# Kernel optimization log

Measured on AMD Instinct MI355X. Metric: run time of the kernel, lower is better.

Reference implementation:

```python
import jax, jax.numpy as jnp
import numpy as np

LOG_2PI = 1.8378770664093453  # log(2*pi)

B, N_FEAT = 4096, 1024
R, K, D = 64, 32, 16  # n_regions, n_batch (distributions per region), region size


def setup_inputs() -> dict:
    key = jax.random.key(0)
    k1, k2, k3, k4 = jax.random.split(key, 4)
    x = jax.random.normal(k1, (B, N_FEAT), dtype=jnp.float32)
    # Regions: partition-like index sets over the feature space (equal size D).
    regions = jax.random.randint(k2, (R, D), 0, N_FEAT, dtype=jnp.int64)
    # Per-region diag-Gaussian params (means ~ N(0, 0.1), scales near 1.0).
    means = 0.1 * jax.random.normal(k3, (R, K, D), dtype=jnp.float32)
    scales = 0.9 + 0.2 * jax.random.uniform(k4, (R, K, D), dtype=jnp.float32)
    return {"x": x, "regions": regions, "means": means, "scales": scales}


def reference(x, regions, means, scales):
    # Gather per-region features in one shot: [B, R, D]
    xg = x[:, regions]
    # Diag-Gaussian log-prob, broadcast over the K distributions per region.
    # z: [B, R, K, D]
    z = (xg[:, :, None, :] - means[None]) / scales[None]
    log_det = jnp.sum(jnp.log(scales), axis=-1)  # [R, K]
    ll = -0.5 * jnp.sum(z * z, axis=-1) - log_det[None] - 0.5 * D * LOG_2PI
    return ll  # [B, R, K] == stack over regions of MVNDiag.log_prob
```

## Files before the change

### kernel.cpp

```cpp
#include <hip/hip_runtime.h>

typedef __attribute__((ext_vector_type(8))) short short8;
typedef __attribute__((ext_vector_type(4))) float floatx4;

#define NB 4096
#define NF 1024
#define NR 64
#define NK 32
#define ND 16
#define HALF_D_LOG2PI 14.702988531274762f

__device__ __forceinline__ unsigned f2bf_bits(float f) {
    unsigned u = __float_as_uint(f);
    return (u + 0x7fffu + ((u >> 16) & 1u)) >> 16;
}
__device__ __forceinline__ float bf_bits2f(unsigned b) {
    return __uint_as_float(b << 16);
}

__global__ __launch_bounds__(256) void prep_kernel(
    const float* __restrict__ means, const float* __restrict__ scales,
    unsigned short* __restrict__ wfrag, float* __restrict__ cv)
{
    int p = blockIdx.x * 256 + threadIdx.x;
    if (p >= NR * NK) return;
    int n  = p & 15;
    int nt = (p >> 4) & 1;
    int r  = p >> 5;

    const float* m = means  + (size_t)p * ND;
    const float* s = scales + (size_t)p * ND;
    float Av[ND], Bv[ND];
    float csum = 0.f;
#pragma unroll
    for (int d = 0; d < ND; ++d) {
        float sd = s[d], md = m[d];
        float a  = 1.0f / sd;
        float a2 = a * a;
        Av[d] = -0.5f * a2;
        Bv[d] = md * a2;
        float c = md * a;
        csum += -0.5f * c * c - logf(sd);
    }
    cv[p] = csum - HALF_D_LOG2PI;

#pragma unroll
    for (int slot = 0; slot < 4; ++slot) {
        int ks = slot >> 1;
#pragma unroll
        for (int d = 0; d < ND; ++d) {
            int Kin  = (slot & 1) * 16 + d;
            int quad = Kin >> 3;
            int j    = Kin & 7;
            int lane = quad * 16 + n;
            size_t idx = ((((size_t)r * 2 + ks) * 2 + nt) * 64 + lane) * 8 + j;
            float v = (slot < 2) ? Av[d] : Bv[d];
            wfrag[idx] = (unsigned short)f2bf_bits(v);
        }
    }
}

__global__ __launch_bounds__(256, 2) void fused_kernel(
    const float* __restrict__ x, const int* __restrict__ regions,
    const unsigned short* __restrict__ wfrag, const float* __restrict__ cv,
    float* __restrict__ out)
{
    __shared__ __align__(16) char lds[16 * 1028 * 4 + 32 * 17 * 4];
    float* xs = (float*)lds;
    int*   ridx = (int*)(lds + 16 * 1028 * 4);
    unsigned short* xg = (unsigned short*)lds;

    const int t  = threadIdx.x;
    const int bt = blockIdx.x;
    const int r0 = blockIdx.y * 32;
    const int b0 = bt * 16;

    for (int j = t; j < 32 * ND; j += 256) {
        int rl = j >> 4, d = j & 15;
        ridx[rl * 17 + d] = regions[(r0 + rl) * ND + d];
    }
    {
        const float4* src = (const float4*)(x + (size_t)b0 * NF);
#pragma unroll
        for (int i = 0; i < 16; ++i)
            *(float4*)(xs + i * 1028 + t * 4) = src[i * 256 + t];
    }
    __syncthreads();

    const int rl = t & 31;
    const int bA = t >> 5;
    int idxv[ND];
#pragma unroll
    for (int d = 0; d < ND; ++d) idxv[d] = ridx[rl * 17 + d];

    unsigned pk[2][32];
#pragma unroll
    for (int pp = 0; pp < 2; ++pp) {
        const int b = bA + pp * 8;
#pragma unroll
        for (int d = 0; d < ND; d += 2) {
            float x0 = xs[b * 1028 + idxv[d]];
            float x1 = xs[b * 1028 + idxv[d + 1]];
            float q0 = x0 * x0, q1 = x1 * x1;
            unsigned h20 = f2bf_bits(q0), h21 = f2bf_bits(q1);
            unsigned l20 = f2bf_bits(q0 - bf_bits2f(h20));
            unsigned l21 = f2bf_bits(q1 - bf_bits2f(h21));
            unsigned h0  = f2bf_bits(x0), h1 = f2bf_bits(x1);
            unsigned l0  = f2bf_bits(x0 - bf_bits2f(h0));
            unsigned l1  = f2bf_bits(x1 - bf_bits2f(h1));
            int di = d >> 1;
            pk[pp][di]      = h20 | (h21 << 16);
            pk[pp][8 + di]  = l20 | (l21 << 16);
            pk[pp][16 + di] = h0  | (h1 << 16);
            pk[pp][24 + di] = l0  | (l1 << 16);
        }
    }
    __syncthreads();

    const int wv   = t >> 6;
    const int L    = t & 63;
    const int m    = L & 15;
    const int quad = L >> 4;
    const short* wfs = (const short*)wfrag;

#pragma unroll
    for (int c = 0; c < 2; ++c) {
        if ((rl >> 4) == c) {
            int rr = rl & 15;
#pragma unroll
            for (int pp = 0; pp < 2; ++pp) {
                int b = bA + pp * 8;
                uint4* d4 = (uint4*)(xg + (rr * 16 + b) * 72);
#pragma unroll
                for (int q = 0; q < 8; ++q) d4[q] = ((uint4*)pk[pp])[q];
            }
        }
        __syncthreads();

#pragma unroll
        for (int i = 0; i < 4; ++i) {
            int rloc = wv * 4 + i;
            int r    = r0 + c * 16 + rloc;
            const unsigned short* arow = xg + (rloc * 16 + m) * 72;
            short8 a0 = *(const short8*)(arow + quad * 8);
            short8 a1 = *(const short8*)(arow + 32 + quad * 8);

            size_t wb = ((size_t)r * 4) * 512 + (size_t)L * 8;
            short8 w00 = *(const short8*)(wfs + wb);
            short8 w01 = *(const short8*)(wfs + wb + 512);
            short8 w10 = *(const short8*)(wfs + wb + 1024);
            short8 w11 = *(const short8*)(wfs + wb + 1536);

            floatx4 acc0 = {0.f, 0.f, 0.f, 0.f};
            floatx4 acc1 = {0.f, 0.f, 0.f, 0.f};
            acc0 = __builtin_amdgcn_mfma_f32_16x16x32_bf16(a0, w00, acc0, 0, 0, 0);
            acc0 = __builtin_amdgcn_mfma_f32_16x16x32_bf16(a1, w10, acc0, 0, 0, 0);
            acc1 = __builtin_amdgcn_mfma_f32_16x16x32_bf16(a0, w01, acc1, 0, 0, 0);
            acc1 = __builtin_amdgcn_mfma_f32_16x16x32_bf16(a1, w11, acc1, 0, 0, 0);

            float c0 = cv[r * NK + m];
            float c1 = cv[r * NK + 16 + m];
            int brow = bt * 16 + quad * 4;
#pragma unroll
            for (int g = 0; g < 4; ++g) {
                size_t ob = (size_t)(brow + g) * (NR * NK) + (size_t)r * NK;
                out[ob + m]      = acc0[g] + c0;
                out[ob + 16 + m] = acc1[g] + c1;
            }
        }
        __syncthreads();
    }
}

extern "C" void kernel_launch(void* const* d_in, const int* in_sizes, int n_in,
                              void* d_out, int out_size, void* d_ws, size_t ws_size,
                              hipStream_t stream) {
    const float* x       = (const float*)d_in[0];
    const int*   regions = (const int*)d_in[1];
    const float* means   = (const float*)d_in[2];
    const float* scales  = (const float*)d_in[3];
    float* out = (float*)d_out;

    char* ws = (char*)d_ws;
    unsigned short* wfrag = (unsigned short*)ws;
    float*          cvp   = (float*)(ws + 262144);

    prep_kernel<<<dim3((NR * NK + 255) / 256), 256, 0, stream>>>(means, scales, wfrag, cvp);
    fused_kernel<<<dim3(NB / 16, 2), 256, 0, stream>>>(x, regions, wfrag, cvp, out);
}
```

Baseline: 90.00 us.

## Parallelize weight prep per region and swizzle single-pass LDS staging

The prep kernel now uses one block per region, staging A/B coefficients in shared memory, reducing the constant term cooperatively and writing the bf16 MFMA fragments as 16-byte vectors instead of scattered 2-byte stores. The fused kernel enlarges its LDS buffer so all 32 regions' gathered features are staged at once, removing the two-chunk loop and its extra barriers. Rows use an XOR swizzle to cut LDS bank conflicts on fragment reads. The larger LDS footprint may limit occupancy, and since the kernel is likely bound by output bandwidth the benefit may be limited.

```diff
diff --git a/kernel.cpp b/kernel.cpp
--- a/kernel.cpp
+++ b/kernel.cpp
@@ -22,42 +22,55 @@
     const float* __restrict__ means, const float* __restrict__ scales,
     unsigned short* __restrict__ wfrag, float* __restrict__ cv)
 {
-    int p = blockIdx.x * 256 + threadIdx.x;
-    if (p >= NR * NK) return;
-    int n  = p & 15;
-    int nt = (p >> 4) & 1;
-    int r  = p >> 5;
-
-    const float* m = means  + (size_t)p * ND;
-    const float* s = scales + (size_t)p * ND;
-    float Av[ND], Bv[ND];
-    float csum = 0.f;
-#pragma unroll
-    for (int d = 0; d < ND; ++d) {
-        float sd = s[d], md = m[d];
-        float a  = 1.0f / sd;
-        float a2 = a * a;
-        Av[d] = -0.5f * a2;
-        Bv[d] = md * a2;
-        float c = md * a;
-        csum += -0.5f * c * c - logf(sd);
-    }
-    cv[p] = csum - HALF_D_LOG2PI;
-
-#pragma unroll
-    for (int slot = 0; slot < 4; ++slot) {
-        int ks = slot >> 1;
-#pragma unroll
-        for (int d = 0; d < ND; ++d) {
-            int Kin  = (slot & 1) * 16 + d;
-            int quad = Kin >> 3;
-            int j    = Kin & 7;
-            int lane = quad * 16 + n;
-            size_t idx = ((((size_t)r * 2 + ks) * 2 + nt) * 64 + lane) * 8 + j;
-            float v = (slot < 2) ? Av[d] : Bv[d];
-            wfrag[idx] = (unsigned short)f2bf_bits(v);
-        }
-    }
+    __shared__ float Asm[NK][ND];
+    __shared__ float Bsm[NK][ND];
+    __shared__ float csum[NK][8];
+    const int r = blockIdx.x;
+    const int t = threadIdx.x;
+
+    {
+        int k  = t >> 3;
+        int d0 = (t & 7) * 2;
+        const float* m = means  + ((size_t)r * NK + k) * ND + d0;
+        const float* s = scales + ((size_t)r * NK + k) * ND + d0;
+        float partial = 0.f;
+#pragma unroll
+        for (int q = 0; q < 2; ++q) {
+            float sd = s[q], md = m[q];
+            float a  = 1.f / sd;
+            float a2 = a * a;
+            Asm[k][d0 + q] = -0.5f * a2;
+            Bsm[k][d0 + q] = md * a2;
+            float c = md * a;
+            partial += -0.5f * c * c - logf(sd);
+        }
+        csum[k][t & 7] = partial;
+    }
+    __syncthreads();
+    if (t < NK) {
+        float acc = 0.f;
+#pragma unroll
+        for (int q = 0; q < 8; ++q) acc += csum[t][q];
+        cv[r * NK + t] = acc - HALF_D_LOG2PI;
+    }
+
+    const int ks   = t >> 7;
+    const int nt   = (t >> 6) & 1;
+    const int lane = t & 63;
+    const int n    = lane & 15;
+    const int qd   = lane >> 4;
+    const int kk   = nt * 16 + n;
+    unsigned px[4];
+#pragma unroll
+    for (int j2 = 0; j2 < 4; ++j2) {
+        int j  = j2 * 2;
+        int d0 = (qd * 8 + j) & 15;
+        int d1 = (qd * 8 + j + 1) & 15;
+        float v0 = ks ? Bsm[kk][d0] : Asm[kk][d0];
+        float v1 = ks ? Bsm[kk][d1] : Asm[kk][d1];
+        px[j2] = f2bf_bits(v0) | (f2bf_bits(v1) << 16);
+    }
+    *(uint4*)(wfrag + ((((size_t)r * 2 + ks) * 2 + nt) * 64 + lane) * 8) = *(uint4*)px;
 }
 
 __global__ __launch_bounds__(256, 2) void fused_kernel(
@@ -65,8 +78,8 @@
     const unsigned short* __restrict__ wfrag, const float* __restrict__ cv,
     float* __restrict__ out)
 {
-    __shared__ __align__(16) char lds[16 * 1028 * 4 + 32 * 17 * 4];
-    float* xs = (float*)lds;
+    __shared__ __align__(16) char lds[73728];
+    float* xs   = (float*)lds;
     int*   ridx = (int*)(lds + 16 * 1028 * 4);
     unsigned short* xg = (unsigned short*)lds;
 
@@ -76,8 +89,8 @@
     const int b0 = bt * 16;
 
     for (int j = t; j < 32 * ND; j += 256) {
-        int rl = j >> 4, d = j & 15;
-        ridx[rl * 17 + d] = regions[(r0 + rl) * ND + d];
+        int rr = j >> 4, d = j & 15;
+        ridx[rr * 17 + d] = regions[(r0 + rr) * ND + d];
     }
     {
         const float4* src = (const float4*)(x + (size_t)b0 * NF);
@@ -117,58 +130,58 @@
     }
     __syncthreads();
 
+    {
+        const int s = rl & 7;
+#pragma unroll
+        for (int pp = 0; pp < 2; ++pp) {
+            int row = rl * 16 + bA + pp * 8;
+            uint4* base = (uint4*)(xg + row * 72);
+#pragma unroll
+            for (int q = 0; q < 8; ++q) base[q ^ s] = ((uint4*)pk[pp])[q];
+        }
+    }
+    __syncthreads();
+
     const int wv   = t >> 6;
     const int L    = t & 63;
-    const int m    = L & 15;
+    const int col  = L & 15;
     const int quad = L >> 4;
     const short* wfs = (const short*)wfrag;
 
-#pragma unroll
-    for (int c = 0; c < 2; ++c) {
-        if ((rl >> 4) == c) {
-            int rr = rl & 15;
-#pragma unroll
-            for (int pp = 0; pp < 2; ++pp) {
-                int b = bA + pp * 8;
-                uint4* d4 = (uint4*)(xg + (rr * 16 + b) * 72);
-#pragma unroll
-                for (int q = 0; q < 8; ++q) d4[q] = ((uint4*)pk[pp])[q];
-            }
-        }
-        __syncthreads();
-
-#pragma unroll
-        for (int i = 0; i < 4; ++i) {
-            int rloc = wv * 4 + i;
-            int r    = r0 + c * 16 + rloc;
-            const unsigned short* arow = xg + (rloc * 16 + m) * 72;
-            short8 a0 = *(const short8*)(arow + quad * 8);
-            short8 a1 = *(const short8*)(arow + 32 + quad * 8);
-
-            size_t wb = ((size_t)r * 4) * 512 + (size_t)L * 8;
-            short8 w00 = *(const short8*)(wfs + wb);
-            short8 w01 = *(const short8*)(wfs + wb + 512);
-            short8 w10 = *(const short8*)(wfs + wb + 1024);
-            short8 w11 = *(const short8*)(wfs + wb + 1536);
-
-            floatx4 acc0 = {0.f, 0.f, 0.f, 0.f};
-            floatx4 acc1 = {0.f, 0.f, 0.f, 0.f};
-            acc0 = __builtin_amdgcn_mfma_f32_16x16x32_bf16(a0, w00, acc0, 0, 0, 0);
-            acc0 = __builtin_amdgcn_mfma_f32_16x16x32_bf16(a1, w10, acc0, 0, 0, 0);
-            acc1 = __builtin_amdgcn_mfma_f32_16x16x32_bf16(a0, w01, acc1, 0, 0, 0);
-            acc1 = __builtin_amdgcn_mfma_f32_16x16x32_bf16(a1, w11, acc1, 0, 0, 0);
-
-            float c0 = cv[r * NK + m];
-            float c1 = cv[r * NK + 16 + m];
-            int brow = bt * 16 + quad * 4;
-#pragma unroll
-            for (int g = 0; g < 4; ++g) {
-                size_t ob = (size_t)(brow + g) * (NR * NK) + (size_t)r * NK;
-                out[ob + m]      = acc0[g] + c0;
-                out[ob + 16 + m] = acc1[g] + c1;
-            }
-        }
-        __syncthreads();
+#pragma unroll 2
+    for (int i = 0; i < 8; ++i) {
+        int rloc = wv * 8 + i;
+        int r    = r0 + rloc;
+        int row  = rloc * 16 + col;
+        int s    = rloc & 7;
+        const uint4* base = (const uint4*)(xg + row * 72);
+        uint4 ca0 = base[quad ^ s];
+        uint4 ca1 = base[(4 + quad) ^ s];
+        short8 a0 = *(short8*)&ca0;
+        short8 a1 = *(short8*)&ca1;
+
+        size_t wb = ((size_t)r * 4) * 512 + (size_t)L * 8;
+        short8 w00 = *(const short8*)(wfs + wb);
+        short8 w01 = *(const short8*)(wfs + wb + 512);
+        short8 w10 = *(const short8*)(wfs + wb + 1024);
+        short8 w11 = *(const short8*)(wfs + wb + 1536);
+
+        floatx4 acc0 = {0.f, 0.f, 0.f, 0.f};
+        floatx4 acc1 = {0.f, 0.f, 0.f, 0.f};
+        acc0 = __builtin_amdgcn_mfma_f32_16x16x32_bf16(a0, w00, acc0, 0, 0, 0);
+        acc0 = __builtin_amdgcn_mfma_f32_16x16x32_bf16(a1, w10, acc0, 0, 0, 0);
+        acc1 = __builtin_amdgcn_mfma_f32_16x16x32_bf16(a0, w01, acc1, 0, 0, 0);
+        acc1 = __builtin_amdgcn_mfma_f32_16x16x32_bf16(a1, w11, acc1, 0, 0, 0);
+
+        float c0 = cv[r * NK + col];
+        float c1 = cv[r * NK + 16 + col];
+        int brow = bt * 16 + quad * 4;
+#pragma unroll
+        for (int g = 0; g < 4; ++g) {
+            size_t ob = (size_t)(brow + g) * (NR * NK) + (size_t)r * NK;
+            out[ob + col]      = acc0[g] + c0;
+            out[ob + 16 + col] = acc1[g] + c1;
+        }
     }
 }
 
@@ -185,6 +198,6 @@
     unsigned short* wfrag = (unsigned short*)ws;
     float*          cvp   = (float*)(ws + 262144);
 
-    prep_kernel<<<dim3((NR * NK + 255) / 256), 256, 0, stream>>>(means, scales, wfrag, cvp);
+    prep_kernel<<<dim3(NR), 256, 0, stream>>>(means, scales, wfrag, cvp);
     fused_kernel<<<dim3(NB / 16, 2), 256, 0, stream>>>(x, regions, wfrag, cvp, out);
 }
```

Measured after the change: 85.56 us. -4.9%, faster.
